# Optimization experiments

Hardware: AMD Instinct MI355X
Metric: run time of the kernel (lower is better)

The kernel has to match this reference:

```python
import jax, jax.numpy as jnp
import numpy as np

N_NODES = 50000
N_EDGES = 800000
D_IN = 96
HID = 96
D_OUT = 64
NUM_LAYERS = 6  # conv1 + (NUM_LAYERS-2) hidden convs + out_conv


def gcn_conv(x, W, b, src, dst, n):
    """PyG GCNConv: add self-loops, symmetric D^-1/2 (A+I) D^-1/2 normalization."""
    h = x @ W  # [n, out_dim]
    loops = jnp.arange(n, dtype=src.dtype)
    s = jnp.concatenate([src, loops])
    d = jnp.concatenate([dst, loops])
    deg = jax.ops.segment_sum(jnp.ones_like(s, dtype=h.dtype), d, num_segments=n)
    dinv = jnp.where(deg > 0, jax.lax.rsqrt(deg), 0.0)
    norm = dinv[s] * dinv[d]                 # [E+n]
    msg = h[s] * norm[:, None]               # gather + scale
    out = jax.ops.segment_sum(msg, d, num_segments=n)  # scatter-add to targets
    return out + b


def setup_inputs() -> dict:
    key = jax.random.key(0)
    ks = jax.random.split(key, 10)
    x = jax.random.normal(ks[0], (N_NODES, D_IN), dtype=jnp.float32)
    edge_index = jax.random.randint(ks[1], (2, N_EDGES), 0, N_NODES, dtype=jnp.int32)
    ricci_curvature = jax.random.normal(ks[2], (N_EDGES,), dtype=jnp.float32)
    n_hidden = NUM_LAYERS - 2
    W1 = jax.random.normal(ks[3], (D_IN, HID), dtype=jnp.float32) * 0.05
    b1 = jnp.zeros((HID,), dtype=jnp.float32)
    Ws = jax.random.normal(ks[4], (n_hidden, HID, HID), dtype=jnp.float32) * 0.05
    bs = jnp.zeros((n_hidden, HID), dtype=jnp.float32)
    Wout = jax.random.normal(ks[5], ((NUM_LAYERS - 1) * HID, D_OUT), dtype=jnp.float32) * 0.05
    bout = jnp.zeros((D_OUT,), dtype=jnp.float32)
    return {
        "x": x, "edge_index": edge_index, "percent": 70,
        "ricci_curvature": ricci_curvature,
        "W1": W1, "b1": b1, "Ws": Ws, "bs": bs, "Wout": Wout, "bout": bout,
    }


def reference(x, edge_index, percent, ricci_curvature, W1, b1, Ws, bs, Wout, bout):
    # Eval path: no sampling / dynamic reweighting, dropout is identity, no BN.
    del percent, ricci_curvature
    n = x.shape[0]
    src, dst = edge_index[0], edge_index[1]
    res = []
    h = jax.nn.relu(gcn_conv(x, W1, b1, src, dst, n))
    res.append(h)
    for i in range(Ws.shape[0]):
        h = jax.nn.relu(gcn_conv(h, Ws[i], bs[i], src, dst, n))
        res.append(h)
    x_cat = jnp.concatenate(res, axis=1)  # JK concatenation: [n, (L-1)*HID]
    out = gcn_conv(x_cat, Wout, bout, src, dst, n)
    return (out,) + tuple(res)
```

## Files before the change

### kernel.cpp

```cpp
#include <hip/hip_runtime.h>


typedef unsigned short ushortT;
typedef __attribute__((ext_vector_type(8))) short bf16x8;
typedef __attribute__((ext_vector_type(4))) float f32x4;

__device__ __forceinline__ ushortT f2b(float f) {
    union { float f; unsigned int u; } v;
    v.f = f;
    unsigned int lsb = (v.u >> 16) & 1u;
    v.u += 0x7fffu + lsb;
    return (ushortT)(v.u >> 16);
}
__device__ __forceinline__ float b2f(ushortT u) {
    union { float f; unsigned int u; } v;
    v.u = ((unsigned int)u) << 16;
    return v.f;
}

__global__ void prep_kernel(const float* __restrict__ W1, const float* __restrict__ Wsl,
                            const float* __restrict__ Wout, ushortT* __restrict__ wt1,
                            ushortT* __restrict__ wts, ushortT* __restrict__ wto,
                            int* __restrict__ degi, int n) {
    const int SQ = 96 * 96;
    const int T1 = 5 * SQ;
    const int T2 = T1 + 480 * 64;
    int i = blockIdx.x * blockDim.x + threadIdx.x;
    if (i < T1) {
        int l = i / SQ, j = i - l * SQ;
        int c = j / 96, k = j - c * 96;
        if (l == 0)
            wt1[j] = f2b(W1[k * 96 + c]);
        else
            wts[(size_t)(l - 1) * SQ + j] = f2b(Wsl[(size_t)(l - 1) * SQ + k * 96 + c]);
    } else if (i < T2) {
        int j = i - T1;
        int c = j / 480, k = j - c * 480;
        wto[j] = f2b(Wout[(size_t)k * 64 + c]);
    } else {
        int j = i - T2;
        if (j < n) degi[j] = 0;
    }
}

__global__ void count_kernel(const int* __restrict__ dst, int* __restrict__ degi, int E) {
    int e = blockIdx.x * blockDim.x + threadIdx.x;
    if (e < E) atomicAdd(&degi[dst[e]], 1);
}

__global__ __launch_bounds__(1024) void scan123(const int* __restrict__ degi,
                                                int* __restrict__ row_start,
                                                float* __restrict__ dinv, int n, int E) {
    __shared__ int tmp[1024];
    const int t = threadIdx.x;
    const int C = (n + 1023) / 1024;
    const int i0 = t * C;
    const int i1 = min(i0 + C, n);
    int s = 0;
    for (int i = i0; i < i1; ++i) s += degi[i];
    tmp[t] = s;
    __syncthreads();
    for (int off = 1; off < 1024; off <<= 1) {
        int v = (t >= off) ? tmp[t - off] : 0;
        __syncthreads();
        tmp[t] += v;
        __syncthreads();
    }
    int base = tmp[t] - s;
    for (int i = i0; i < i1; ++i) {
        const int d = degi[i];
        row_start[i] = base;
        dinv[i] = rsqrtf((float)d + 1.0f);
        base += d;
    }
    if (t == 1023) row_start[n] = E;
}

__global__ __launch_bounds__(256) void fill_gemm1(
        const int* __restrict__ src, const int* __restrict__ dst,
        const int* __restrict__ row_start, int* __restrict__ degi,
        int* __restrict__ col, int E, int gF,
        const float* __restrict__ X, const ushortT* __restrict__ Wt,
        const float* __restrict__ dinv, ushortT* __restrict__ g, int n) {
    if (blockIdx.x < gF) {
        int e = blockIdx.x * blockDim.x + threadIdx.x;
        if (e < E) {
            int d = dst[e];
            int pos = row_start[d] + atomicSub(&degi[d], 1) - 1;
            col[pos] = src[e];
        }
        return;
    }
    __shared__ __attribute__((aligned(16))) ushortT Xl[64][104];
    __shared__ __attribute__((aligned(16))) ushortT Wtl[96][104];
    const int tid = threadIdx.x;
    const int wave = tid >> 6, lane = tid & 63;
    const int quad = lane >> 4, m = lane & 15;
    const int row_base = (blockIdx.x - gF) * 64;
    for (int i = tid; i < 96 * 24; i += 256) {
        int r = i / 24, c4 = (i % 24) * 4;
        *(ushort4*)&Wtl[r][c4] = *(const ushort4*)&Wt[r * 96 + c4];
    }
    for (int i = tid; i < 64 * 24; i += 256) {
        int r = i / 24, c4 = (i % 24) * 4;
        int grow = min(row_base + r, n - 1);
        float4 v = *(const float4*)&X[(size_t)grow * 96 + c4];
        ushort4 o = {f2b(v.x), f2b(v.y), f2b(v.z), f2b(v.w)};
        *(ushort4*)&Xl[r][c4] = o;
    }
    __syncthreads();
    f32x4 acc[6] = {};
#pragma unroll
    for (int ks = 0; ks < 3; ++ks) {
        bf16x8 a = *(bf16x8*)&Xl[wave * 16 + m][ks * 32 + quad * 8];
#pragma unroll
        for (int ct = 0; ct < 6; ++ct) {
            bf16x8 b = *(bf16x8*)&Wtl[ct * 16 + m][ks * 32 + quad * 8];
            acc[ct] = __builtin_amdgcn_mfma_f32_16x16x32_bf16(a, b, acc[ct], 0, 0, 0);
        }
    }
    float di[4];
    int rows[4];
#pragma unroll
    for (int r = 0; r < 4; ++r) {
        rows[r] = row_base + wave * 16 + quad * 4 + r;
        di[r] = (rows[r] < n) ? dinv[rows[r]] : 0.f;
    }
#pragma unroll
    for (int ct = 0; ct < 6; ++ct) {
        int colx = ct * 16 + m;
#pragma unroll
        for (int r = 0; r < 4; ++r)
            if (rows[r] < n) g[(size_t)rows[r] * 96 + colx] = f2b(acc[ct][r] * di[r]);
    }
}

template <typename TIN>
__global__ __launch_bounds__(256) void gemm96_mfma(const TIN* __restrict__ X,
                                                   const ushortT* __restrict__ Wt,
                                                   const float* __restrict__ dinv,
                                                   ushortT* __restrict__ g, int n) {
    __shared__ __attribute__((aligned(16))) ushortT Xl[64][104];
    __shared__ __attribute__((aligned(16))) ushortT Wtl[96][104];
    const int tid = threadIdx.x;
    const int wave = tid >> 6, lane = tid & 63;
    const int quad = lane >> 4, m = lane & 15;
    const int row_base = blockIdx.x * 64;
    for (int i = tid; i < 96 * 24; i += 256) {
        int r = i / 24, c4 = (i % 24) * 4;
        *(ushort4*)&Wtl[r][c4] = *(const ushort4*)&Wt[r * 96 + c4];
    }
    for (int i = tid; i < 64 * 24; i += 256) {
        int r = i / 24, c4 = (i % 24) * 4;
        int grow = min(row_base + r, n - 1);
        if constexpr (sizeof(TIN) == 4) {
            float4 v = *(const float4*)&X[(size_t)grow * 96 + c4];
            ushort4 o = {f2b(v.x), f2b(v.y), f2b(v.z), f2b(v.w)};
            *(ushort4*)&Xl[r][c4] = o;
        } else {
            *(ushort4*)&Xl[r][c4] = *(const ushort4*)&X[(size_t)grow * 96 + c4];
        }
    }
    __syncthreads();
    f32x4 acc[6] = {};
#pragma unroll
    for (int ks = 0; ks < 3; ++ks) {
        bf16x8 a = *(bf16x8*)&Xl[wave * 16 + m][ks * 32 + quad * 8];
#pragma unroll
        for (int ct = 0; ct < 6; ++ct) {
            bf16x8 b = *(bf16x8*)&Wtl[ct * 16 + m][ks * 32 + quad * 8];
            acc[ct] = __builtin_amdgcn_mfma_f32_16x16x32_bf16(a, b, acc[ct], 0, 0, 0);
        }
    }
    float di[4];
    int rows[4];
#pragma unroll
    for (int r = 0; r < 4; ++r) {
        rows[r] = row_base + wave * 16 + quad * 4 + r;
        di[r] = (rows[r] < n) ? dinv[rows[r]] : 0.f;
    }
#pragma unroll
    for (int ct = 0; ct < 6; ++ct) {
        int colx = ct * 16 + m;
#pragma unroll
        for (int r = 0; r < 4; ++r)
            if (rows[r] < n) g[(size_t)rows[r] * 96 + colx] = f2b(acc[ct][r] * di[r]);
    }
}

template <typename TIN>
__global__ __launch_bounds__(256) void gemm_out_mfma(const TIN* __restrict__ hcat,
                                                     const ushortT* __restrict__ Wt,
                                                     const float* __restrict__ dinv,
                                                     ushortT* __restrict__ g, int n) {
    __shared__ __attribute__((aligned(16))) ushortT Xl[64][104];
    __shared__ __attribute__((aligned(16))) ushortT Wtl[64][104];
    const int tid = threadIdx.x;
    const int wave = tid >> 6, lane = tid & 63;
    const int quad = lane >> 4, m = lane & 15;
    const int row_base = blockIdx.x * 64;
    f32x4 acc[4] = {};
    for (int seg = 0; seg < 5; ++seg) {
        const TIN* hl = hcat + (size_t)seg * (size_t)n * 96;
        __syncthreads();
        for (int i = tid; i < 64 * 24; i += 256) {
            int r = i / 24, c4 = (i % 24) * 4;
            *(ushort4*)&Wtl[r][c4] = *(const ushort4*)&Wt[r * 480 + seg * 96 + c4];
        }
        for (int i = tid; i < 64 * 24; i += 256) {
            int r = i / 24, c4 = (i % 24) * 4;
            int grow = min(row_base + r, n - 1);
            if constexpr (sizeof(TIN) == 4) {
                float4 v = *(const float4*)&hl[(size_t)grow * 96 + c4];
                ushort4 o = {f2b(v.x), f2b(v.y), f2b(v.z), f2b(v.w)};
                *(ushort4*)&Xl[r][c4] = o;
            } else {
                *(ushort4*)&Xl[r][c4] = *(const ushort4*)&hl[(size_t)grow * 96 + c4];
            }
        }
        __syncthreads();
#pragma unroll
        for (int ks = 0; ks < 3; ++ks) {
            bf16x8 a = *(bf16x8*)&Xl[wave * 16 + m][ks * 32 + quad * 8];
#pragma unroll
            for (int ct = 0; ct < 4; ++ct) {
                bf16x8 b = *(bf16x8*)&Wtl[ct * 16 + m][ks * 32 + quad * 8];
                acc[ct] = __builtin_amdgcn_mfma_f32_16x16x32_bf16(a, b, acc[ct], 0, 0, 0);
            }
        }
    }
    float di[4];
    int rows[4];
#pragma unroll
    for (int r = 0; r < 4; ++r) {
        rows[r] = row_base + wave * 16 + quad * 4 + r;
        di[r] = (rows[r] < n) ? dinv[rows[r]] : 0.f;
    }
#pragma unroll
    for (int ct = 0; ct < 4; ++ct) {
        int colx = ct * 16 + m;
#pragma unroll
        for (int r = 0; r < 4; ++r)
            if (rows[r] < n) g[(size_t)rows[r] * 64 + colx] = f2b(acc[ct][r] * di[r]);
    }
}

template <int F, bool RELU, bool WRITE_BF16>
__global__ void agg_csr(const int* __restrict__ row_start, const int* __restrict__ col,
                        const ushortT* __restrict__ g, const float* __restrict__ dinv,
                        const float* __restrict__ b, float* __restrict__ out,
                        ushortT* __restrict__ hb, int n) {
    constexpr int NV = F / 4;
    const int lane = threadIdx.x & 63;
    const int half = lane >> 5;
    const int l32 = lane & 31;
    const int v = blockIdx.x * (blockDim.x >> 6) + (threadIdx.x >> 6);
    if (v >= n) return;
    const int e0 = row_start[v];
    const int e1 = row_start[v + 1];
    const bool act = (l32 < NV);
    const size_t fo = (size_t)l32 * 4;
    float a0 = 0.f, a1 = 0.f, a2 = 0.f, a3 = 0.f;
    float s0 = 0.f, s1 = 0.f, s2 = 0.f, s3 = 0.f;
    if (half == 0 && act) {
        ushort4 s = *(const ushort4*)&g[(size_t)v * F + fo];
        a0 = b2f(s.x); a1 = b2f(s.y); a2 = b2f(s.z); a3 = b2f(s.w);
    }
    const int total = e1 - e0;
    const int cntH = (total - half + 1) >> 1;
    const int base = e0 + half;
    const int sb = half << 5;
    int done = 0;
    while (done < cntH) {
        const int kc = min(cntH - done, 32);
        int cv = 0;
        if (l32 < kc) cv = col[base + 2 * (done + l32)];
        int j = 0;
        for (; j + 8 <= kc; j += 8) {
            int c0 = __shfl(cv, sb + j + 0);
            int c1 = __shfl(cv, sb + j + 1);
            int c2 = __shfl(cv, sb + j + 2);
            int c3 = __shfl(cv, sb + j + 3);
            int c4 = __shfl(cv, sb + j + 4);
            int c5 = __shfl(cv, sb + j + 5);
            int c6 = __shfl(cv, sb + j + 6);
            int c7 = __shfl(cv, sb + j + 7);
            if (act) {
                ushort4 g0 = *(const ushort4*)&g[(size_t)c0 * F + fo];
                ushort4 g1 = *(const ushort4*)&g[(size_t)c1 * F + fo];
                ushort4 g2 = *(const ushort4*)&g[(size_t)c2 * F + fo];
                ushort4 g3 = *(const ushort4*)&g[(size_t)c3 * F + fo];
                ushort4 g4 = *(const ushort4*)&g[(size_t)c4 * F + fo];
                ushort4 g5 = *(const ushort4*)&g[(size_t)c5 * F + fo];
                ushort4 g6 = *(const ushort4*)&g[(size_t)c6 * F + fo];
                ushort4 g7 = *(const ushort4*)&g[(size_t)c7 * F + fo];
                a0 += (b2f(g0.x) + b2f(g1.x)) + (b2f(g2.x) + b2f(g3.x));
                a1 += (b2f(g0.y) + b2f(g1.y)) + (b2f(g2.y) + b2f(g3.y));
                a2 += (b2f(g0.z) + b2f(g1.z)) + (b2f(g2.z) + b2f(g3.z));
                a3 += (b2f(g0.w) + b2f(g1.w)) + (b2f(g2.w) + b2f(g3.w));
                s0 += (b2f(g4.x) + b2f(g5.x)) + (b2f(g6.x) + b2f(g7.x));
                s1 += (b2f(g4.y) + b2f(g5.y)) + (b2f(g6.y) + b2f(g7.y));
                s2 += (b2f(g4.z) + b2f(g5.z)) + (b2f(g6.z) + b2f(g7.z));
                s3 += (b2f(g4.w) + b2f(g5.w)) + (b2f(g6.w) + b2f(g7.w));
            }
        }
        if (j + 4 <= kc) {
            int c0 = __shfl(cv, sb + j + 0);
            int c1 = __shfl(cv, sb + j + 1);
            int c2 = __shfl(cv, sb + j + 2);
            int c3 = __shfl(cv, sb + j + 3);
            if (act) {
                ushort4 g0 = *(const ushort4*)&g[(size_t)c0 * F + fo];
                ushort4 g1 = *(const ushort4*)&g[(size_t)c1 * F + fo];
                ushort4 g2 = *(const ushort4*)&g[(size_t)c2 * F + fo];
                ushort4 g3 = *(const ushort4*)&g[(size_t)c3 * F + fo];
                a0 += b2f(g0.x) + b2f(g1.x);
                a1 += b2f(g0.y) + b2f(g1.y);
                a2 += b2f(g0.z) + b2f(g1.z);
                a3 += b2f(g0.w) + b2f(g1.w);
                s0 += b2f(g2.x) + b2f(g3.x);
                s1 += b2f(g2.y) + b2f(g3.y);
                s2 += b2f(g2.z) + b2f(g3.z);
                s3 += b2f(g2.w) + b2f(g3.w);
            }
            j += 4;
        }
        if (j + 2 <= kc) {
            int c0 = __shfl(cv, sb + j + 0);
            int c1 = __shfl(cv, sb + j + 1);
            if (act) {
                ushort4 g0 = *(const ushort4*)&g[(size_t)c0 * F + fo];
                ushort4 g1 = *(const ushort4*)&g[(size_t)c1 * F + fo];
                a0 += b2f(g0.x) + b2f(g1.x);
                a1 += b2f(g0.y) + b2f(g1.y);
                a2 += b2f(g0.z) + b2f(g1.z);
                a3 += b2f(g0.w) + b2f(g1.w);
            }
            j += 2;
        }
        if (j < kc) {
            int c0 = __shfl(cv, sb + j);
            if (act) {
                ushort4 g0 = *(const ushort4*)&g[(size_t)c0 * F + fo];
                a0 += b2f(g0.x); a1 += b2f(g0.y); a2 += b2f(g0.z); a3 += b2f(g0.w);
            }
        }
        done += kc;
    }
    a0 += s0; a1 += s1; a2 += s2; a3 += s3;
    a0 += __shfl_xor(a0, 32);
    a1 += __shfl_xor(a1, 32);
    a2 += __shfl_xor(a2, 32);
    a3 += __shfl_xor(a3, 32);
    if (half == 0 && act) {
        const float di = dinv[v];
        const float4 bv = *(const float4*)&b[l32 * 4];
        float4 r;
        r.x = a0 * di + bv.x;
        r.y = a1 * di + bv.y;
        r.z = a2 * di + bv.z;
        r.w = a3 * di + bv.w;
        if (RELU) {
            r.x = fmaxf(r.x, 0.f); r.y = fmaxf(r.y, 0.f);
            r.z = fmaxf(r.z, 0.f); r.w = fmaxf(r.w, 0.f);
        }
        *(float4*)&out[(size_t)v * F + l32 * 4] = r;
        if (WRITE_BF16) {
            ushort4 o = {f2b(r.x), f2b(r.y), f2b(r.z), f2b(r.w)};
            *(ushort4*)&hb[(size_t)v * F + l32 * 4] = o;
        }
    }
}

extern "C" void kernel_launch(void* const* d_in, const int* in_sizes, int n_in,
                              void* d_out, int out_size, void* d_ws, size_t ws_size,
                              hipStream_t stream) {
    const float* x    = (const float*)d_in[0];
    const int*   ei   = (const int*)d_in[1];
    const float* W1   = (const float*)d_in[4];
    const float* b1   = (const float*)d_in[5];
    const float* Wsl  = (const float*)d_in[6];
    const float* bsl  = (const float*)d_in[7];
    const float* Wout = (const float*)d_in[8];
    const float* bout = (const float*)d_in[9];

    const int n = in_sizes[0] / 96;
    const int E = in_sizes[1] / 2;
    const int* src = ei;
    const int* dst = ei + E;

    char* p = (char*)d_ws;
    int*     degi      = (int*)p;              p += (size_t)n * 4;
    int*     row_start = (int*)p;              p += (size_t)(n + 1) * 4;
    int*     partials  = (int*)p;              p += 256 * 4;
    int*     col       = (int*)p;              p += (size_t)E * 4;
    float*   dinv      = (float*)p;            p += (size_t)n * 4;
    ushortT* g         = (ushortT*)p;          p += (size_t)n * 96 * 2;
    ushortT* hball     = (ushortT*)p;
    const size_t wbytes = (size_t)(5 * 9216 + 30720) * 2;
    const size_t fixed  = (size_t)(p - (char*)d_ws);
    const bool   big    = (fixed + (size_t)5 * n * 96 * 2 + wbytes) <= ws_size;
    const size_t hbsz   = big ? (size_t)5 * n * 96 : (size_t)n * 96;
    p += hbsz * 2;
    ushortT* wt1 = (ushortT*)p;
    ushortT* wts = wt1 + 9216;
    ushortT* wto = wts + 4 * 9216;
    (void)partials;

    float* out  = (float*)d_out;
    float* hseg = out + (size_t)n * 64;

    const int nthr = 256;
    const int gE   = (E + nthr - 1) / nthr;
    const int gAgg = (n + 3) / 4;
    const int gT64 = (n + 63) / 64;

    const int prep_items = 76800 + n;
    prep_kernel<<<(prep_items + 255) / 256, 256, 0, stream>>>(W1, Wsl, Wout, wt1, wts,
                                                              wto, degi, n);

    count_kernel<<<gE, nthr, 0, stream>>>(dst, degi, E);
    scan123<<<1, 1024, 0, stream>>>(degi, row_start, dinv, n, E);
    fill_gemm1<<<gE + gT64, nthr, 0, stream>>>(src, dst, row_start, degi, col, E, gE,
                                               x, wt1, dinv, g, n);

    agg_csr<96, true, true><<<gAgg, nthr, 0, stream>>>(row_start, col, g, dinv, b1,
                                                       hseg, hball, n);

    for (int l = 0; l < 4; ++l) {
        float*   hnext = hseg + (size_t)(l + 1) * (size_t)n * 96;
        ushortT* hbin  = big ? (hball + (size_t)l * n * 96) : hball;
        ushortT* hbout = big ? (hball + (size_t)(l + 1) * n * 96) : hball;
        gemm96_mfma<ushortT><<<gT64, 256, 0, stream>>>(hbin, wts + (size_t)l * 9216,
                                                       dinv, g, n);
        agg_csr<96, true, true><<<gAgg, nthr, 0, stream>>>(row_start, col, g, dinv,
                                                           bsl + (size_t)l * 96, hnext,
                                                           hbout, n);
    }

    if (big)
        gemm_out_mfma<ushortT><<<gT64, 256, 0, stream>>>(hball, wto, dinv, g, n);
    else
        gemm_out_mfma<float><<<gT64, 256, 0, stream>>>(hseg, wto, dinv, g, n);
    agg_csr<64, false, false><<<gAgg, nthr, 0, stream>>>(row_start, col, g, dinv, bout,
                                                         out, nullptr, n);
}
```

Measured before the change: 609.6 us.

## Replace single-block degree scan with three-pass multi-block scan; fuse prep with counting

The CSR row-offset scan, which ran in one 1024-thread block looping serially over ~49 nodes per thread, becomes a three-kernel multi-block scan: per-block scans, a scan of the block partials, then a fix-up pass that also computes dinv. Weight conversion and edge-degree counting are merged into one launch, and degree zeroing moves to a hipMemsetAsync. This is meant to remove the serial single-block bottleneck and one launch, at the cost of extra launches for the scan passes. scan2 only handles up to 256 partials, which is enough for 50000 nodes (196 blocks).

```diff
diff --git a/kernel.cpp b/kernel.cpp
--- a/kernel.cpp
+++ b/kernel.cpp
@@ -18,62 +18,76 @@
     return v.f;
 }
 
-__global__ void prep_kernel(const float* __restrict__ W1, const float* __restrict__ Wsl,
-                            const float* __restrict__ Wout, ushortT* __restrict__ wt1,
-                            ushortT* __restrict__ wts, ushortT* __restrict__ wto,
-                            int* __restrict__ degi, int n) {
+__global__ void prep_count(const float* __restrict__ W1, const float* __restrict__ Wsl,
+                           const float* __restrict__ Wout, ushortT* __restrict__ wt1,
+                           ushortT* __restrict__ wts, ushortT* __restrict__ wto,
+                           const int* __restrict__ dst, int* __restrict__ degi,
+                           int E, int gP) {
     const int SQ = 96 * 96;
     const int T1 = 5 * SQ;
     const int T2 = T1 + 480 * 64;
-    int i = blockIdx.x * blockDim.x + threadIdx.x;
-    if (i < T1) {
-        int l = i / SQ, j = i - l * SQ;
-        int c = j / 96, k = j - c * 96;
-        if (l == 0)
-            wt1[j] = f2b(W1[k * 96 + c]);
-        else
-            wts[(size_t)(l - 1) * SQ + j] = f2b(Wsl[(size_t)(l - 1) * SQ + k * 96 + c]);
-    } else if (i < T2) {
-        int j = i - T1;
-        int c = j / 480, k = j - c * 480;
-        wto[j] = f2b(Wout[(size_t)k * 64 + c]);
+    if (blockIdx.x < gP) {
+        int i = blockIdx.x * blockDim.x + threadIdx.x;
+        if (i < T1) {
+            int l = i / SQ, j = i - l * SQ;
+            int c = j / 96, k = j - c * 96;
+            if (l == 0)
+                wt1[j] = f2b(W1[k * 96 + c]);
+            else
+                wts[(size_t)(l - 1) * SQ + j] = f2b(Wsl[(size_t)(l - 1) * SQ + k * 96 + c]);
+        } else if (i < T2) {
+            int j = i - T1;
+            int c = j / 480, k = j - c * 480;
+            wto[j] = f2b(Wout[(size_t)k * 64 + c]);
+        }
     } else {
-        int j = i - T2;
-        if (j < n) degi[j] = 0;
-    }
-}
-
-__global__ void count_kernel(const int* __restrict__ dst, int* __restrict__ degi, int E) {
-    int e = blockIdx.x * blockDim.x + threadIdx.x;
-    if (e < E) atomicAdd(&degi[dst[e]], 1);
-}
-
-__global__ __launch_bounds__(1024) void scan123(const int* __restrict__ degi,
-                                                int* __restrict__ row_start,
-                                                float* __restrict__ dinv, int n, int E) {
-    __shared__ int tmp[1024];
+        int e = (blockIdx.x - gP) * blockDim.x + threadIdx.x;
+        if (e < E) atomicAdd(&degi[dst[e]], 1);
+    }
+}
+
+__global__ void scan1(const int* __restrict__ degi, int* __restrict__ row_start,
+                      int* __restrict__ partials, int n) {
+    __shared__ int tmp[256];
     const int t = threadIdx.x;
-    const int C = (n + 1023) / 1024;
-    const int i0 = t * C;
-    const int i1 = min(i0 + C, n);
-    int s = 0;
-    for (int i = i0; i < i1; ++i) s += degi[i];
-    tmp[t] = s;
+    const int i = blockIdx.x * 256 + t;
+    int val = (i < n) ? degi[i] : 0;
+    tmp[t] = val;
     __syncthreads();
-    for (int off = 1; off < 1024; off <<= 1) {
+    for (int off = 1; off < 256; off <<= 1) {
         int v = (t >= off) ? tmp[t - off] : 0;
         __syncthreads();
         tmp[t] += v;
         __syncthreads();
     }
-    int base = tmp[t] - s;
-    for (int i = i0; i < i1; ++i) {
-        const int d = degi[i];
-        row_start[i] = base;
-        dinv[i] = rsqrtf((float)d + 1.0f);
-        base += d;
-    }
-    if (t == 1023) row_start[n] = E;
+    if (i < n) row_start[i] = tmp[t] - val;
+    if (t == 255) partials[blockIdx.x] = tmp[255];
+}
+
+__global__ void scan2(int* __restrict__ partials, int nb) {
+    __shared__ int tmp[256];
+    const int t = threadIdx.x;
+    int val = (t < nb) ? partials[t] : 0;
+    tmp[t] = val;
+    __syncthreads();
+    for (int off = 1; off < 256; off <<= 1) {
+        int v = (t >= off) ? tmp[t - off] : 0;
+        __syncthreads();
+        tmp[t] += v;
+        __syncthreads();
+    }
+    if (t < nb) partials[t] = tmp[t] - val;
+}
+
+__global__ void scan3(const int* __restrict__ degi, int* __restrict__ row_start,
+                      const int* __restrict__ partials, float* __restrict__ dinv,
+                      int n, int E) {
+    const int i = blockIdx.x * 256 + threadIdx.x;
+    if (i < n) {
+        row_start[i] += partials[blockIdx.x];
+        dinv[i] = rsqrtf((float)degi[i] + 1.0f);
+    }
+    if (i == 0) row_start[n] = E;
 }
 
 __global__ __launch_bounds__(256) void fill_gemm1(
@@ -405,7 +419,6 @@
     ushortT* wt1 = (ushortT*)p;
     ushortT* wts = wt1 + 9216;
     ushortT* wto = wts + 4 * 9216;
-    (void)partials;
 
     float* out  = (float*)d_out;
     float* hseg = out + (size_t)n * 64;
@@ -414,13 +427,17 @@
     const int gE   = (E + nthr - 1) / nthr;
     const int gAgg = (n + 3) / 4;
     const int gT64 = (n + 63) / 64;
-
-    const int prep_items = 76800 + n;
-    prep_kernel<<<(prep_items + 255) / 256, 256, 0, stream>>>(W1, Wsl, Wout, wt1, wts,
-                                                              wto, degi, n);
-
-    count_kernel<<<gE, nthr, 0, stream>>>(dst, degi, E);
-    scan123<<<1, 1024, 0, stream>>>(degi, row_start, dinv, n, E);
+    const int nb   = (n + 255) / 256;
+    const int gP   = (76800 + 255) / 256;
+
+    hipMemsetAsync(degi, 0, (size_t)n * sizeof(int), stream);
+    prep_count<<<gP + gE, nthr, 0, stream>>>(W1, Wsl, Wout, wt1, wts, wto,
+                                             dst, degi, E, gP);
+
+    scan1<<<nb, 256, 0, stream>>>(degi, row_start, partials, n);
+    scan2<<<1, 256, 0, stream>>>(partials, nb);
+    scan3<<<nb, 256, 0, stream>>>(degi, row_start, partials, dinv, n, E);
+
     fill_gemm1<<<gE + gT64, nthr, 0, stream>>>(src, dst, row_start, degi, col, E, gE,
                                                x, wt1, dinv, g, n);
 
```

Result: faster. 512.2 us (-16.0%).
